# Optimization experiments

Measured on AMD Instinct MI355X. Metric: run time of the kernel, lower is better.

Reference implementation:

```python
import jax, jax.numpy as jnp
import numpy as np
from jax import lax

# config: B=8, T=32, input_chans=1, H=kernel_size=8, W=n_freq=256
# F1=32, F2=48, F3=256, F4=128, n_note=88, pooling_size=2, filter_size3=(3,64)
B, T, CIN, H, W = 8, 32, 1, 8, 256
F1, F2, F3, F4, NNOTE = 32, 48, 256, 128, 88


def _conv2d(x, w, b, padding):
    # x: (B, Cin, H, W), w: (Cout, Cin, kh, kw)
    y = lax.conv_general_dilated(x, w, (1, 1), padding,
                                 dimension_numbers=('NCHW', 'OIHW', 'NCHW'))
    return y + b[None, :, None, None]


def _clstm(x, w, b, F):
    # x: (B, C, T, H, W); ConvLSTM (no peephole, no LN), 'same' padding.
    xs = jnp.moveaxis(x, 2, 0)  # (T, B, C, H, W)
    h0 = jnp.zeros((x.shape[0], F, x.shape[3], x.shape[4]), x.dtype)
    c0 = h0

    def step(carry, xt):
        h, c = carry
        z = _conv2d(jnp.concatenate([xt, h], axis=1), w, b, 'SAME')
        i, f, g, o = jnp.split(z, 4, axis=1)
        c = jax.nn.sigmoid(f) * c + jax.nn.sigmoid(i) * jnp.tanh(g)
        h = jax.nn.sigmoid(o) * jnp.tanh(c)
        return (h, c), h

    _, hs = lax.scan(step, (h0, c0), xs)  # (T, B, F, H, W)
    return jnp.moveaxis(hs, 0, 2)  # (B, F, T, H, W)


def _maxpool3d(x):
    # MaxPool3d(kernel=2, stride=2) over (T, H, W) of a (B, C, T, H, W) tensor
    return lax.reduce_window(x, -jnp.inf, lax.max,
                             (1, 1, 2, 2, 2), (1, 1, 2, 2, 2), 'VALID')


def setup_inputs() -> dict:
    key = jax.random.key(0)
    ks = jax.random.split(key, 11)
    s = 0.05
    return {
        'x':  jax.random.normal(ks[0], (B, CIN, T, H, W), jnp.float32),
        'w1': jax.random.normal(ks[1], (4 * F1, CIN + F1, 3, 3), jnp.float32) * s,
        'b1': jnp.zeros((4 * F1,), jnp.float32),
        'w2': jax.random.normal(ks[2], (4 * F2, F1 + F2, 3, 3), jnp.float32) * s,
        'b2': jnp.zeros((4 * F2,), jnp.float32),
        'w3': jax.random.normal(ks[3], (F3, F2, 3, 64), jnp.float32) * s,
        'b3': jnp.zeros((F3,), jnp.float32),
        'w4': jax.random.normal(ks[4], (F4, F3, 1, 1), jnp.float32) * s,
        'b4': jnp.zeros((F4,), jnp.float32),
        'w5': jax.random.normal(ks[5], (NNOTE, F4, 1, 1), jnp.float32) * s,
        'b5': jnp.zeros((NNOTE,), jnp.float32),
    }


def reference(x, w1, b1, w2, b2, w3, b3, w4, b4, w5, b5):
    x = _clstm(x, w1, b1, F1)          # (B, F1, T, H, W)
    x = _maxpool3d(x)                  # (B, F1, T/2, H/2, W/2)
    x = _clstm(x, w2, b2, F2)          # (B, F2, T/2, H/2, W/2)
    x = _maxpool3d(x)                  # (B, F2, 8, 2, 64)
    x = x.reshape(B, F2, -1, 64)       # (B, F2, 16, 64), filter_size3[1]=64
    x = jax.nn.elu(_conv2d(x, w3, b3, 'VALID'))  # (B, F3, 14, 1); dropout=eval noop
    x = jax.nn.elu(_conv2d(x, w4, b4, 'VALID'))  # (B, F4, 14, 1)
    x = _conv2d(x, w5, b5, 'VALID')              # (B, 88, 14, 1)
    return x
```

## Files before the change

kernel.cpp:

```cpp
#include <hip/hip_runtime.h>
#include <math.h>


#define DEVINL static __device__ __forceinline__
typedef __attribute__((ext_vector_type(8))) short short8;
typedef __attribute__((ext_vector_type(4))) float f32x4;

#define PLANE_W3 2359296

DEVINL float sigm(float x) { return 1.0f / (1.0f + __expf(-x)); }
DEVINL float tanh_fast(float x) { return 1.0f - 2.0f / (__expf(2.0f * x) + 1.0f); }
DEVINL float elu(float x) { return x > 0.0f ? x : expm1f(x); }
DEVINL unsigned short bf16_rne(float v) {
    unsigned u = __float_as_uint(v);
    unsigned r = (u + 0x7FFF + ((u >> 16) & 1)) >> 16;
    return (unsigned short)r;
}
DEVINL float bf16_to_f(unsigned short h) { return __uint_as_float(((unsigned)h) << 16); }
DEVINL unsigned pack_hl(float v) {
    unsigned short hi = bf16_rne(v);
    unsigned short lo = bf16_rne(v - bf16_to_f(hi));
    return (unsigned)hi | ((unsigned)lo << 16);
}
DEVINL float upk(unsigned u) {
    return __uint_as_float(u << 16) + __uint_as_float(u & 0xffff0000u);
}

DEVINL void lstm1_body(
    int xq, int y, int b, int t,
    const unsigned* __restrict__ xpk, const unsigned short* __restrict__ w1F,
    const float* __restrict__ b1,
    const unsigned* __restrict__ hprev, const unsigned* __restrict__ hpool,
    unsigned* __restrict__ hout, float* __restrict__ c1,
    unsigned* __restrict__ p1pk)
{
    __shared__ __align__(16) unsigned short sBhi[34 * 128];
    __shared__ __align__(16) unsigned short sBlo[34 * 128];
    const int x0 = xq * 32;
    const int tid = threadIdx.x;

    if (((t & 1) == 0) && t >= 2 && (y & 1) == 1) {
        int tp = (t >> 1) - 1, yp = y >> 1;
        for (int e = tid; e < 512; e += 256) {
            int f = e >> 4, xl = e & 15;
            int xp = (x0 >> 1) + xl, gx = x0 + 2 * xl;
            int b0 = ((b * 32 + f) * 8 + (y - 1)) * 256 + gx;
            float m = upk(hpool[b0]);
            m = fmaxf(m, upk(hpool[b0 + 1]));
            m = fmaxf(m, upk(hpool[b0 + 256]));
            m = fmaxf(m, upk(hpool[b0 + 257]));
            m = fmaxf(m, upk(hprev[b0]));
            m = fmaxf(m, upk(hprev[b0 + 1]));
            m = fmaxf(m, upk(hprev[b0 + 256]));
            m = fmaxf(m, upk(hprev[b0 + 257]));
            p1pk[(((b * 32 + f) * 16 + tp) * 4 + yp) * 128 + xp] = pack_hl(m);
        }
    }

    for (int e = tid; e < 34 * 128; e += 256) {
        int lx = e % 34, kk = e / 34;
        unsigned u = 0;
        if (kk < 99) {
            int ci = kk / 3, dy = kk - ci * 3;
            int gy = y + dy - 1, gx = x0 + lx - 1;
            if (gy >= 0 && gy < 8 && gx >= 0 && gx < 256)
                u = (ci == 0) ? xpk[((b * 32 + t) * 8 + gy) * 256 + gx]
                              : hprev[((b * 32 + (ci - 1)) * 8 + gy) * 256 + gx];
        }
        int a16 = lx * 128 + (((kk >> 3) ^ (lx & 15)) << 3) + (kk & 7);
        sBhi[a16] = (unsigned short)u;
        sBlo[a16] = (unsigned short)(u >> 16);
    }
    __syncthreads();

    const int l = tid & 63;
    const int wv = __builtin_amdgcn_readfirstlane(tid >> 6);
    const int ln = l & 15, kg = l >> 4;
    f32x4 acc[2][2];
#pragma unroll
    for (int i = 0; i < 2; ++i)
#pragma unroll
        for (int j = 0; j < 2; ++j) acc[i][j] = (f32x4){0.f, 0.f, 0.f, 0.f};

#pragma unroll
    for (int kk = 0; kk < 4; ++kk) {
        short8 bh[2][3], bl[2][3];
#pragma unroll
        for (int ntl = 0; ntl < 2; ++ntl)
#pragma unroll
            for (int dx = 0; dx < 3; ++dx) {
                int lx = ntl * 16 + ln + dx;
                int slot = kk * 4 + kg;
                int boff = lx * 128 + ((slot ^ (lx & 15)) << 3);
                bh[ntl][dx] = *(const short8*)&sBhi[boff];
                bl[ntl][dx] = *(const short8*)&sBlo[boff];
            }
#pragma unroll
        for (int mtl = 0; mtl < 2; ++mtl)
#pragma unroll
            for (int dx = 0; dx < 3; ++dx) {
                int aoff = ((((dx * 8 + wv * 2 + mtl) * 4 + kk) * 4 + kg) * 16 + ln) * 8;
                short8 ah = *(const short8*)&w1F[aoff];
#pragma unroll
                for (int ntl = 0; ntl < 2; ++ntl) {
                    acc[mtl][ntl] = __builtin_amdgcn_mfma_f32_16x16x32_bf16(ah, bl[ntl][dx], acc[mtl][ntl], 0, 0, 0);
                    acc[mtl][ntl] = __builtin_amdgcn_mfma_f32_16x16x32_bf16(ah, bh[ntl][dx], acc[mtl][ntl], 0, 0, 0);
                }
            }
    }

#pragma unroll
    for (int mtl = 0; mtl < 2; ++mtl) {
        const int f = (wv * 2 + mtl) * 4 + kg;
        const float bi = b1[f], bff = b1[32 + f], bg = b1[64 + f], bo = b1[96 + f];
#pragma unroll
        for (int ntl = 0; ntl < 2; ++ntl) {
            f32x4 a = acc[mtl][ntl];
            int gidx = ((b * 32 + f) * 8 + y) * 256 + x0 + ntl * 16 + ln;
            float zi = a[0] + bi, zf = a[1] + bff, zg = a[2] + bg, zo = a[3] + bo;
            float cv = c1[gidx];
            float cn = sigm(zf) * cv + sigm(zi) * tanh_fast(zg);
            c1[gidx] = cn;
            hout[gidx] = pack_hl(sigm(zo) * tanh_fast(cn));
        }
    }
}

DEVINL void lstm2_body(
    int xq, int y, int b, int t,
    const unsigned* __restrict__ p1pk, const unsigned short* __restrict__ w2F,
    const float* __restrict__ b2,
    const unsigned* __restrict__ hprev, const unsigned* __restrict__ hpool,
    float* __restrict__ c2, unsigned* __restrict__ hout,
    unsigned short* __restrict__ p2hi, unsigned short* __restrict__ p2lo,
    const unsigned* __restrict__ h30, const unsigned* __restrict__ h31)
{
    __shared__ __align__(16) unsigned short sChi[18 * 256];
    __shared__ __align__(16) unsigned short sClo[18 * 256];
    const int x0 = xq * 16;
    const int tid = threadIdx.x;

    if (((t & 1) == 0) && t >= 2 && y < 2) {
        int tp = (t >> 1) - 1;
        for (int e = tid; e < 48 * 8; e += 256) {
            int f = e >> 3, xl = e & 7;
            int xp = xq * 8 + xl;
            int g0 = ((b * 48 + f) * 4 + y * 2) * 128 + xp * 2;
            float m = fmaxf(fmaxf(upk(hpool[g0]), upk(hpool[g0 + 1])),
                            fmaxf(upk(hpool[g0 + 128]), upk(hpool[g0 + 129])));
            m = fmaxf(m, fmaxf(fmaxf(upk(hprev[g0]), upk(hprev[g0 + 1])),
                               fmaxf(upk(hprev[g0 + 128]), upk(hprev[g0 + 129]))));
            int pi = ((b * 48 + f) * 16 + tp * 2 + y) * 64 + xp;
            unsigned pm = pack_hl(m);
            p2hi[pi] = (unsigned short)pm;
            p2lo[pi] = (unsigned short)(pm >> 16);
        }
    }

    for (int idx = tid; idx < 80 * 54; idx += 256) {
        int ci = idx / 54, rem = idx % 54;
        int dy = rem / 18, lx = rem % 18;
        int gy = y + dy - 1, gx = x0 + lx - 1;
        unsigned u = 0;
        if (gy >= 0 && gy < 4 && gx >= 0 && gx < 128) {
            if (ci < 32) {
                if (t == 15) {
                    int b0 = ((b * 32 + ci) * 8 + gy * 2) * 256 + gx * 2;
                    float m = upk(h30[b0]);
                    m = fmaxf(m, upk(h30[b0 + 1]));
                    m = fmaxf(m, upk(h30[b0 + 256]));
                    m = fmaxf(m, upk(h30[b0 + 257]));
                    m = fmaxf(m, upk(h31[b0]));
                    m = fmaxf(m, upk(h31[b0 + 1]));
                    m = fmaxf(m, upk(h31[b0 + 256]));
                    m = fmaxf(m, upk(h31[b0 + 257]));
                    u = pack_hl(m);
                } else {
                    u = p1pk[(((b * 32 + ci) * 16 + t) * 4 + gy) * 128 + gx];
                }
            } else {
                u = hprev[((b * 48 + (ci - 32)) * 4 + gy) * 128 + gx];
            }
        }
        int k = ci * 3 + dy;
        int a16 = lx * 256 + (((k >> 3) ^ (lx & 15)) << 3) + (k & 7);
        sChi[a16] = (unsigned short)u;
        sClo[a16] = (unsigned short)(u >> 16);
    }
    for (int e = tid; e < 18 * 16; e += 256) {
        int lx = e >> 4, k = 240 + (e & 15);
        int a16 = lx * 256 + (((k >> 3) ^ (lx & 15)) << 3) + (k & 7);
        sChi[a16] = 0;
        sClo[a16] = 0;
    }
    __syncthreads();

    const int l = tid & 63;
    const int wv = __builtin_amdgcn_readfirstlane(tid >> 6);
    const int ln = l & 15, kg = l >> 4;
    f32x4 acc[3] = {{0.f,0.f,0.f,0.f},{0.f,0.f,0.f,0.f},{0.f,0.f,0.f,0.f}};

#pragma unroll
    for (int kk = 0; kk < 8; ++kk) {
        short8 bh[3], bl[3];
#pragma unroll
        for (int dx = 0; dx < 3; ++dx) {
            int lx = ln + dx;
            int boff = lx * 256 + ((((kk << 2) + kg) ^ (lx & 15)) << 3);
            bh[dx] = *(const short8*)&sChi[boff];
            bl[dx] = *(const short8*)&sClo[boff];
        }
#pragma unroll
        for (int j = 0; j < 3; ++j) {
            int mt = wv * 3 + j;
#pragma unroll
            for (int dx = 0; dx < 3; ++dx) {
                int aoff = ((((dx * 12 + mt) * 8 + kk) * 4 + kg) * 16 + ln) * 8;
                short8 ah = *(const short8*)&w2F[aoff];
                acc[j] = __builtin_amdgcn_mfma_f32_16x16x32_bf16(ah, bl[dx], acc[j], 0, 0, 0);
                acc[j] = __builtin_amdgcn_mfma_f32_16x16x32_bf16(ah, bh[dx], acc[j], 0, 0, 0);
            }
        }
    }

    const int x = x0 + ln;
#pragma unroll
    for (int j = 0; j < 3; ++j) {
        int mt = wv * 3 + j;
        int f = mt * 4 + kg;
        float zi = acc[j][0] + b2[f];
        float zf = acc[j][1] + b2[48 + f];
        float zg = acc[j][2] + b2[96 + f];
        float zo = acc[j][3] + b2[144 + f];
        int gidx = ((b * 48 + f) * 4 + y) * 128 + x;
        float cv = c2[gidx];
        float cn = sigm(zf) * cv + sigm(zi) * tanh_fast(zg);
        c2[gidx] = cn;
        hout[gidx] = pack_hl(sigm(zo) * tanh_fast(cn));
    }
}

__global__ __launch_bounds__(256) void step_k(
    const unsigned* __restrict__ xpk, const unsigned short* __restrict__ w1F,
    const float* __restrict__ b1,
    const unsigned* __restrict__ hprev1, const unsigned* __restrict__ hpool1,
    unsigned* __restrict__ hout1, float* __restrict__ c1,
    unsigned* __restrict__ p1pk,
    const unsigned short* __restrict__ w2F, const float* __restrict__ b2,
    const unsigned* __restrict__ hprev2, const unsigned* __restrict__ hpool2,
    unsigned* __restrict__ hout2, float* __restrict__ c2,
    unsigned short* __restrict__ p2hi, unsigned short* __restrict__ p2lo,
    int t, int t2)
{
    int bid = blockIdx.x;
    if (gridDim.x == 768) {
        if (bid < 256) {
            lstm2_body(bid & 7, (bid >> 3) & 3, bid >> 5, t2,
                       p1pk, w2F, b2, hprev2, hpool2, c2, hout2, p2hi, p2lo,
                       hout1, hout1);
            return;
        }
        bid -= 256;
    }
    lstm1_body(bid & 7, (bid >> 3) & 7, bid >> 6, t,
               xpk, w1F, b1, hprev1, hpool1, hout1, c1, p1pk);
}

__global__ __launch_bounds__(256) void lstm2_k(
    const unsigned* __restrict__ p1pk, const unsigned short* __restrict__ w2F,
    const float* __restrict__ b2,
    const unsigned* __restrict__ hprev, const unsigned* __restrict__ hpool,
    float* __restrict__ c2, unsigned* __restrict__ hout,
    unsigned short* __restrict__ p2hi, unsigned short* __restrict__ p2lo,
    const unsigned* __restrict__ h30, const unsigned* __restrict__ h31, int t)
{
    int bid = blockIdx.x;
    lstm2_body(bid & 7, (bid >> 3) & 3, bid >> 5, t,
               p1pk, w2F, b2, hprev, hpool, c2, hout, p2hi, p2lo, h30, h31);
}

__global__ void pool2(const unsigned* __restrict__ hA, const unsigned* __restrict__ hB,
                      unsigned short* __restrict__ p2hi, unsigned short* __restrict__ p2lo,
                      int tp)
{
    int idx = blockIdx.x * 256 + threadIdx.x;
    if (idx >= 8 * 48 * 2 * 64) return;
    int xp = idx & 63;
    int t1 = idx >> 6;
    int yp = t1 & 1; t1 >>= 1;
    int f = t1 % 48, b = t1 / 48;
    float m = -INFINITY;
#pragma unroll
    for (int dy = 0; dy < 2; ++dy)
#pragma unroll
        for (int dx = 0; dx < 2; ++dx) {
            int g = ((b * 48 + f) * 4 + yp * 2 + dy) * 128 + xp * 2 + dx;
            m = fmaxf(m, fmaxf(upk(hA[g]), upk(hB[g])));
        }
    int pi = ((b * 48 + f) * 16 + tp * 2 + yp) * 64 + xp;
    unsigned pm = pack_hl(m);
    p2hi[pi] = (unsigned short)pm;
    p2lo[pi] = (unsigned short)(pm >> 16);
}

__global__ __launch_bounds__(256) void conv3_part(
    const unsigned short* __restrict__ p2hi, const unsigned short* __restrict__ p2lo,
    const unsigned short* __restrict__ w3F,
    float* __restrict__ part)
{
    __shared__ float sRed[4 * 7 * 256];
    const int mq = blockIdx.x, ck = blockIdx.y;
    const int tid = threadIdx.x;
    const int l = tid & 63;
    const int wv = __builtin_amdgcn_readfirstlane(tid >> 6);
    const int c = ck * 4 + wv;
    const int ln = l & 15, kg = l >> 4;

    int rowbase[7];
#pragma unroll
    for (int nt = 0; nt < 7; ++nt) {
        int col = nt * 16 + ln;
        int bi = col / 14, r = col % 14;
        rowbase[nt] = (bi * 48 + c) * 16 + r;
    }

    f32x4 acc[7];
#pragma unroll
    for (int nt = 0; nt < 7; ++nt) acc[nt] = (f32x4){0.f, 0.f, 0.f, 0.f};

#pragma unroll
    for (int kk = 0; kk < 6; ++kk) {
        int aoff = ((((mq * 48 + c) * 6 + kk) * 4 + kg) * 16 + ln) * 8;
        short8 ah = *(const short8*)&w3F[aoff];
        short8 al = *(const short8*)&w3F[PLANE_W3 + aoff];
        int s = kk * 4 + kg;
        int dr = s >> 3, w0 = (s & 7) * 8;
#pragma unroll
        for (int nt = 0; nt < 7; ++nt) {
            int boff = (rowbase[nt] + dr) * 64 + w0;
            short8 bh = *(const short8*)&p2hi[boff];
            short8 bl = *(const short8*)&p2lo[boff];
            acc[nt] = __builtin_amdgcn_mfma_f32_16x16x32_bf16(al, bh, acc[nt], 0, 0, 0);
            acc[nt] = __builtin_amdgcn_mfma_f32_16x16x32_bf16(ah, bl, acc[nt], 0, 0, 0);
            acc[nt] = __builtin_amdgcn_mfma_f32_16x16x32_bf16(ah, bh, acc[nt], 0, 0, 0);
        }
    }

#pragma unroll
    for (int nt = 0; nt < 7; ++nt)
        *(f32x4*)&sRed[wv * 1792 + nt * 256 + l * 4] = acc[nt];
    __syncthreads();

#pragma unroll
    for (int nt = 0; nt < 7; ++nt) {
        float s = sRed[nt * 256 + tid] + sRed[1792 + nt * 256 + tid] +
                  sRed[2 * 1792 + nt * 256 + tid] + sRed[3 * 1792 + nt * 256 + tid];
        int r16 = (tid >> 6) * 4 + (tid & 3);
        int m = mq * 16 + r16;
        int col = nt * 16 + ((tid >> 2) & 15);
        part[(ck * 256 + m) * 112 + col] = s;
    }
}

__global__ __launch_bounds__(256) void head(
    const float* __restrict__ part, const float* __restrict__ b3,
    const float* __restrict__ w4T, const float* __restrict__ b4,
    const float* __restrict__ w5T, const float* __restrict__ b5,
    float* __restrict__ out)
{
    __shared__ float sO3[256];
    __shared__ float sO4[128];
    const int col = blockIdx.x;
    const int b = col / 14, r = col % 14;
    const int tid = threadIdx.x;

    float s = b3[tid];
#pragma unroll
    for (int ck = 0; ck < 12; ++ck)
        s += part[(ck * 256 + tid) * 112 + col];
    sO3[tid] = elu(s);
    __syncthreads();

    if (tid < 128) {
        float a4 = b4[tid];
        for (int c = 0; c < 256; ++c)
            a4 = fmaf(sO3[c], w4T[c * 128 + tid], a4);
        sO4[tid] = elu(a4);
    }
    __syncthreads();

    if (tid < 88) {
        float a5 = b5[tid];
        for (int c = 0; c < 128; ++c)
            a5 = fmaf(sO4[c], w5T[c * 88 + tid], a5);
        out[(b * 88 + tid) * 14 + r] = a5;
    }
}

__global__ void prep(const float* __restrict__ x, const float* __restrict__ w1,
                     const float* __restrict__ w2, const float* __restrict__ w3,
                     const float* __restrict__ w4, const float* __restrict__ w5,
                     unsigned* __restrict__ zeroA,
                     unsigned* __restrict__ zeroB,
                     unsigned* __restrict__ xpk,
                     unsigned short* __restrict__ w1F, unsigned short* __restrict__ w2F,
                     unsigned short* __restrict__ w3F,
                     float* __restrict__ w4T, float* __restrict__ w5T)
{
    int i = blockIdx.x * 256 + threadIdx.x;
    if (i < 65536) {
        uint4 z = {0, 0, 0, 0};
        uint4* p = (uint4*)&zeroA[i * 16];
        p[0] = z; p[1] = z; p[2] = z; p[3] = z;
        return;
    }
    i -= 65536;
    if (i < 24576) {
        uint4 z = {0, 0, 0, 0};
        uint4* p = (uint4*)&zeroB[i * 16];
        p[0] = z; p[1] = z; p[2] = z; p[3] = z;
        return;
    }
    i -= 24576;
    if (i < 131072) {
        const float4 v = *(const float4*)&x[i * 4];
        uint4 o;
        o.x = pack_hl(v.x); o.y = pack_hl(v.y);
        o.z = pack_hl(v.z); o.w = pack_hl(v.w);
        *(uint4*)&xpk[i * 4] = o;
        return;
    }
    i -= 131072;
    if (i < 6144) {
        int base = i * 8;
        int dx = base / 16384, rem = base % 16384;
        int mt = rem / 2048, r2 = rem % 2048;
        int kk = r2 / 512, r3 = r2 % 512;
        int kg = r3 / 128, ln = (r3 % 128) / 8;
        int f = mt * 4 + (ln >> 2), gate = ln & 3;
        int co = gate * 32 + f;
        int k0 = kk * 32 + kg * 8;
        short8 h;
#pragma unroll
        for (int e = 0; e < 8; ++e) {
            int k = k0 + e;
            float v = (k < 99) ? w1[co * 297 + (k / 3) * 9 + (k % 3) * 3 + dx] : 0.0f;
            h[e] = (short)bf16_rne(v);
        }
        *(short8*)&w1F[base] = h;
        return;
    }
    i -= 6144;
    if (i < 18432) {
        int base = i * 8;
        int dx = base / 49152, rem = base % 49152;
        int mt = rem / 4096, r2 = rem % 4096;
        int kk = r2 / 512, r3 = r2 % 512;
        int kg = r3 / 128, ln = (r3 % 128) / 8;
        int f = mt * 4 + (ln >> 2), gate = ln & 3;
        int co = gate * 48 + f;
        int k0 = kk * 32 + kg * 8;
        short8 h;
#pragma unroll
        for (int e = 0; e < 8; ++e) {
            int k = k0 + e;
            float v = (k < 240) ? w2[co * 720 + (k / 3) * 9 + (k % 3) * 3 + dx] : 0.0f;
            h[e] = (short)bf16_rne(v);
        }
        *(short8*)&w2F[base] = h;
        return;
    }
    i -= 18432;
    if (i < 294912) {
        int base = i * 8;
        int mq = base / 147456, rem = base % 147456;
        int c = rem / 3072, r2 = rem % 3072;
        int kk = r2 / 512, r3 = r2 % 512;
        int kg = r3 / 128, ln = (r3 % 128) / 8;
        int m = mq * 16 + ln;
        int kc0 = kk * 32 + kg * 8;
        int dr = kc0 >> 6, w0 = kc0 & 63;
        const float* src = &w3[((m * 48 + c) * 3 + dr) * 64 + w0];
        short8 hh, hl;
#pragma unroll
        for (int e = 0; e < 8; ++e) {
            float v = src[e];
            unsigned short hi = bf16_rne(v);
            hh[e] = (short)hi;
            hl[e] = (short)bf16_rne(v - bf16_to_f(hi));
        }
        *(short8*)&w3F[base] = hh;
        *(short8*)&w3F[PLANE_W3 + base] = hl;
        return;
    }
    i -= 294912;
    if (i < 32768) {
        int n = i / 256, cch = i % 256;
        w4T[cch * 128 + n] = w4[i];
        return;
    }
    i -= 32768;
    if (i < 11264) {
        int n = i / 128, cch = i % 128;
        w5T[cch * 88 + n] = w5[i];
    }
}

extern "C" void kernel_launch(void* const* d_in, const int* in_sizes, int n_in,
                              void* d_out, int out_size, void* d_ws, size_t ws_size,
                              hipStream_t stream)
{
    const float* x  = (const float*)d_in[0];
    const float* w1 = (const float*)d_in[1];
    const float* b1 = (const float*)d_in[2];
    const float* w2 = (const float*)d_in[3];
    const float* b2 = (const float*)d_in[4];
    const float* w3 = (const float*)d_in[5];
    const float* b3 = (const float*)d_in[6];
    const float* w4 = (const float*)d_in[7];
    const float* b4 = (const float*)d_in[8];
    const float* w5 = (const float*)d_in[9];
    const float* b5 = (const float*)d_in[10];
    float* out = (float*)d_out;

    float* ws = (float*)d_ws;
    size_t off = 0;
    auto alloc = [&](size_t n) { float* p = ws + off; off += n; return p; };
    unsigned* h1[3];
    h1[0] = (unsigned*)alloc(524288); h1[1] = (unsigned*)alloc(524288);
    h1[2] = (unsigned*)alloc(524288);
    float* c1 = alloc(524288);
    unsigned* xpk = (unsigned*)alloc(524288);
    unsigned* p1pk = (unsigned*)alloc(2097152);
    unsigned* h2[3];
    h2[0] = (unsigned*)alloc(196608); h2[1] = (unsigned*)alloc(196608);
    h2[2] = (unsigned*)alloc(196608);
    float* c2 = alloc(196608);
    unsigned short* p2hi = (unsigned short*)alloc(196608);
    unsigned short* p2lo = (unsigned short*)alloc(196608);
    float* part = alloc(344064);
    unsigned short* w1F = (unsigned short*)alloc(24576);
    unsigned short* w2F = (unsigned short*)alloc(73728);
    unsigned short* w3F = (unsigned short*)alloc(2359296);
    float* w4T = alloc(32768);
    float* w5T = alloc(11264);
    (void)ws_size; (void)off;

    prep<<<2284, 256, 0, stream>>>(x, w1, w2, w3, w4, w5,
                                   h1[2], h2[2], xpk, w1F, w2F, w3F, w4T, w5T);

    for (int t = 0; t < 32; ++t) {
        int t2 = ((t & 1) == 0 && t >= 4) ? (t - 4) / 2 : (t == 31 ? 14 : -1);
        int nblk = (t2 >= 0) ? 768 : 512;
        step_k<<<nblk, 256, 0, stream>>>(
            xpk, w1F, b1, h1[(t + 2) % 3], h1[(t + 1) % 3], h1[t % 3], c1, p1pk,
            w2F, b2,
            t2 >= 0 ? h2[(t2 + 2) % 3] : h2[0],
            t2 >= 0 ? h2[(t2 + 1) % 3] : h2[0],
            t2 >= 0 ? h2[t2 % 3] : h2[0],
            c2, p2hi, p2lo, t, t2);
    }

    lstm2_k<<<256, 256, 0, stream>>>(p1pk, w2F, b2, h2[2], h2[1], c2, h2[0],
                                     p2hi, p2lo, h1[0], h1[1], 15);
    pool2<<<192, 256, 0, stream>>>(h2[2], h2[0], p2hi, p2lo, 7);

    conv3_part<<<dim3(16, 12), 256, 0, stream>>>(p2hi, p2lo, w3F, part);
    head<<<112, 256, 0, stream>>>(part, b3, w4T, b4, w5T, b5, out);
}
```

Baseline: 484.6 us.

## Fold weight prep into first LSTM step and drop state zeroing and x packing

The big prep kernel is split up. A tiny prep1 packs only w1, and the w2/w3/w4/w5 repacking runs as extra blocks of the t=0 step kernel, overlapping the first LSTM1 step. The zero-fill of the h/c buffers is removed: at t=0 the code skips hprev loads and treats c as zero. The input x is now hi/lo-split on the fly inside the LSTM1 tile load instead of through a precomputed xpk buffer. This removes a serial prep launch and memory traffic, at the cost of extra pack work every step and a larger t=0 grid.

After: 505.3 us. 1.04x slower.

```diff
diff --git a/kernel.cpp b/kernel.cpp
--- a/kernel.cpp
+++ b/kernel.cpp
@@ -28,7 +28,7 @@
 
 DEVINL void lstm1_body(
     int xq, int y, int b, int t,
-    const unsigned* __restrict__ xpk, const unsigned short* __restrict__ w1F,
+    const float* __restrict__ x, const unsigned short* __restrict__ w1F,
     const float* __restrict__ b1,
     const unsigned* __restrict__ hprev, const unsigned* __restrict__ hpool,
     unsigned* __restrict__ hout, float* __restrict__ c1,
@@ -63,9 +63,12 @@
         if (kk < 99) {
             int ci = kk / 3, dy = kk - ci * 3;
             int gy = y + dy - 1, gx = x0 + lx - 1;
-            if (gy >= 0 && gy < 8 && gx >= 0 && gx < 256)
-                u = (ci == 0) ? xpk[((b * 32 + t) * 8 + gy) * 256 + gx]
-                              : hprev[((b * 32 + (ci - 1)) * 8 + gy) * 256 + gx];
+            if (gy >= 0 && gy < 8 && gx >= 0 && gx < 256) {
+                if (ci == 0)
+                    u = pack_hl(x[((b * 32 + t) * 8 + gy) * 256 + gx]);
+                else if (t > 0)
+                    u = hprev[((b * 32 + (ci - 1)) * 8 + gy) * 256 + gx];
+            }
         }
         int a16 = lx * 128 + (((kk >> 3) ^ (lx & 15)) << 3) + (kk & 7);
         sBhi[a16] = (unsigned short)u;
@@ -118,7 +121,7 @@
             f32x4 a = acc[mtl][ntl];
             int gidx = ((b * 32 + f) * 8 + y) * 256 + x0 + ntl * 16 + ln;
             float zi = a[0] + bi, zf = a[1] + bff, zg = a[2] + bg, zo = a[3] + bo;
-            float cv = c1[gidx];
+            float cv = (t > 0) ? c1[gidx] : 0.0f;
             float cn = sigm(zf) * cv + sigm(zi) * tanh_fast(zg);
             c1[gidx] = cn;
             hout[gidx] = pack_hl(sigm(zo) * tanh_fast(cn));
@@ -178,7 +181,7 @@
                 } else {
                     u = p1pk[(((b * 32 + ci) * 16 + t) * 4 + gy) * 128 + gx];
                 }
-            } else {
+            } else if (t > 0) {
                 u = hprev[((b * 48 + (ci - 32)) * 4 + gy) * 128 + gx];
             }
         }
@@ -233,226 +236,22 @@
         float zg = acc[j][2] + b2[96 + f];
         float zo = acc[j][3] + b2[144 + f];
         int gidx = ((b * 48 + f) * 4 + y) * 128 + x;
-        float cv = c2[gidx];
+        float cv = (t > 0) ? c2[gidx] : 0.0f;
         float cn = sigm(zf) * cv + sigm(zi) * tanh_fast(zg);
         c2[gidx] = cn;
         hout[gidx] = pack_hl(sigm(zo) * tanh_fast(cn));
     }
 }
 
-__global__ __launch_bounds__(256) void step_k(
-    const unsigned* __restrict__ xpk, const unsigned short* __restrict__ w1F,
-    const float* __restrict__ b1,
-    const unsigned* __restrict__ hprev1, const unsigned* __restrict__ hpool1,
-    unsigned* __restrict__ hout1, float* __restrict__ c1,
-    unsigned* __restrict__ p1pk,
-    const unsigned short* __restrict__ w2F, const float* __restrict__ b2,
-    const unsigned* __restrict__ hprev2, const unsigned* __restrict__ hpool2,
-    unsigned* __restrict__ hout2, float* __restrict__ c2,
-    unsigned short* __restrict__ p2hi, unsigned short* __restrict__ p2lo,
-    int t, int t2)
-{
-    int bid = blockIdx.x;
-    if (gridDim.x == 768) {
-        if (bid < 256) {
-            lstm2_body(bid & 7, (bid >> 3) & 3, bid >> 5, t2,
-                       p1pk, w2F, b2, hprev2, hpool2, c2, hout2, p2hi, p2lo,
-                       hout1, hout1);
-            return;
-        }
-        bid -= 256;
-    }
-    lstm1_body(bid & 7, (bid >> 3) & 7, bid >> 6, t,
-               xpk, w1F, b1, hprev1, hpool1, hout1, c1, p1pk);
-}
-
-__global__ __launch_bounds__(256) void lstm2_k(
-    const unsigned* __restrict__ p1pk, const unsigned short* __restrict__ w2F,
-    const float* __restrict__ b2,
-    const unsigned* __restrict__ hprev, const unsigned* __restrict__ hpool,
-    float* __restrict__ c2, unsigned* __restrict__ hout,
-    unsigned short* __restrict__ p2hi, unsigned short* __restrict__ p2lo,
-    const unsigned* __restrict__ h30, const unsigned* __restrict__ h31, int t)
-{
-    int bid = blockIdx.x;
-    lstm2_body(bid & 7, (bid >> 3) & 3, bid >> 5, t,
-               p1pk, w2F, b2, hprev, hpool, c2, hout, p2hi, p2lo, h30, h31);
-}
-
-__global__ void pool2(const unsigned* __restrict__ hA, const unsigned* __restrict__ hB,
-                      unsigned short* __restrict__ p2hi, unsigned short* __restrict__ p2lo,
-                      int tp)
-{
-    int idx = blockIdx.x * 256 + threadIdx.x;
-    if (idx >= 8 * 48 * 2 * 64) return;
-    int xp = idx & 63;
-    int t1 = idx >> 6;
-    int yp = t1 & 1; t1 >>= 1;
-    int f = t1 % 48, b = t1 / 48;
-    float m = -INFINITY;
-#pragma unroll
-    for (int dy = 0; dy < 2; ++dy)
-#pragma unroll
-        for (int dx = 0; dx < 2; ++dx) {
-            int g = ((b * 48 + f) * 4 + yp * 2 + dy) * 128 + xp * 2 + dx;
-            m = fmaxf(m, fmaxf(upk(hA[g]), upk(hB[g])));
-        }
-    int pi = ((b * 48 + f) * 16 + tp * 2 + yp) * 64 + xp;
-    unsigned pm = pack_hl(m);
-    p2hi[pi] = (unsigned short)pm;
-    p2lo[pi] = (unsigned short)(pm >> 16);
-}
-
-__global__ __launch_bounds__(256) void conv3_part(
-    const unsigned short* __restrict__ p2hi, const unsigned short* __restrict__ p2lo,
-    const unsigned short* __restrict__ w3F,
-    float* __restrict__ part)
-{
-    __shared__ float sRed[4 * 7 * 256];
-    const int mq = blockIdx.x, ck = blockIdx.y;
-    const int tid = threadIdx.x;
-    const int l = tid & 63;
-    const int wv = __builtin_amdgcn_readfirstlane(tid >> 6);
-    const int c = ck * 4 + wv;
-    const int ln = l & 15, kg = l >> 4;
-
-    int rowbase[7];
-#pragma unroll
-    for (int nt = 0; nt < 7; ++nt) {
-        int col = nt * 16 + ln;
-        int bi = col / 14, r = col % 14;
-        rowbase[nt] = (bi * 48 + c) * 16 + r;
-    }
-
-    f32x4 acc[7];
-#pragma unroll
-    for (int nt = 0; nt < 7; ++nt) acc[nt] = (f32x4){0.f, 0.f, 0.f, 0.f};
-
-#pragma unroll
-    for (int kk = 0; kk < 6; ++kk) {
-        int aoff = ((((mq * 48 + c) * 6 + kk) * 4 + kg) * 16 + ln) * 8;
-        short8 ah = *(const short8*)&w3F[aoff];
-        short8 al = *(const short8*)&w3F[PLANE_W3 + aoff];
-        int s = kk * 4 + kg;
-        int dr = s >> 3, w0 = (s & 7) * 8;
-#pragma unroll
-        for (int nt = 0; nt < 7; ++nt) {
-            int boff = (rowbase[nt] + dr) * 64 + w0;
-            short8 bh = *(const short8*)&p2hi[boff];
-            short8 bl = *(const short8*)&p2lo[boff];
-            acc[nt] = __builtin_amdgcn_mfma_f32_16x16x32_bf16(al, bh, acc[nt], 0, 0, 0);
-            acc[nt] = __builtin_amdgcn_mfma_f32_16x16x32_bf16(ah, bl, acc[nt], 0, 0, 0);
-            acc[nt] = __builtin_amdgcn_mfma_f32_16x16x32_bf16(ah, bh, acc[nt], 0, 0, 0);
-        }
-    }
-
-#pragma unroll
-    for (int nt = 0; nt < 7; ++nt)
-        *(f32x4*)&sRed[wv * 1792 + nt * 256 + l * 4] = acc[nt];
-    __syncthreads();
-
-#pragma unroll
-    for (int nt = 0; nt < 7; ++nt) {
-        float s = sRed[nt * 256 + tid] + sRed[1792 + nt * 256 + tid] +
-                  sRed[2 * 1792 + nt * 256 + tid] + sRed[3 * 1792 + nt * 256 + tid];
-        int r16 = (tid >> 6) * 4 + (tid & 3);
-        int m = mq * 16 + r16;
-        int col = nt * 16 + ((tid >> 2) & 15);
-        part[(ck * 256 + m) * 112 + col] = s;
-    }
-}
-
-__global__ __launch_bounds__(256) void head(
-    const float* __restrict__ part, const float* __restrict__ b3,
-    const float* __restrict__ w4T, const float* __restrict__ b4,
-    const float* __restrict__ w5T, const float* __restrict__ b5,
-    float* __restrict__ out)
-{
-    __shared__ float sO3[256];
-    __shared__ float sO4[128];
-    const int col = blockIdx.x;
-    const int b = col / 14, r = col % 14;
-    const int tid = threadIdx.x;
-
-    float s = b3[tid];
-#pragma unroll
-    for (int ck = 0; ck < 12; ++ck)
-        s += part[(ck * 256 + tid) * 112 + col];
-    sO3[tid] = elu(s);
-    __syncthreads();
-
-    if (tid < 128) {
-        float a4 = b4[tid];
-        for (int c = 0; c < 256; ++c)
-            a4 = fmaf(sO3[c], w4T[c * 128 + tid], a4);
-        sO4[tid] = elu(a4);
-    }
-    __syncthreads();
-
-    if (tid < 88) {
-        float a5 = b5[tid];
-        for (int c = 0; c < 128; ++c)
-            a5 = fmaf(sO4[c], w5T[c * 88 + tid], a5);
-        out[(b * 88 + tid) * 14 + r] = a5;
-    }
-}
-
-__global__ void prep(const float* __restrict__ x, const float* __restrict__ w1,
-                     const float* __restrict__ w2, const float* __restrict__ w3,
-                     const float* __restrict__ w4, const float* __restrict__ w5,
-                     unsigned* __restrict__ zeroA,
-                     unsigned* __restrict__ zeroB,
-                     unsigned* __restrict__ xpk,
-                     unsigned short* __restrict__ w1F, unsigned short* __restrict__ w2F,
-                     unsigned short* __restrict__ w3F,
-                     float* __restrict__ w4T, float* __restrict__ w5T)
-{
-    int i = blockIdx.x * 256 + threadIdx.x;
-    if (i < 65536) {
-        uint4 z = {0, 0, 0, 0};
-        uint4* p = (uint4*)&zeroA[i * 16];
-        p[0] = z; p[1] = z; p[2] = z; p[3] = z;
-        return;
-    }
-    i -= 65536;
-    if (i < 24576) {
-        uint4 z = {0, 0, 0, 0};
-        uint4* p = (uint4*)&zeroB[i * 16];
-        p[0] = z; p[1] = z; p[2] = z; p[3] = z;
-        return;
-    }
-    i -= 24576;
-    if (i < 131072) {
-        const float4 v = *(const float4*)&x[i * 4];
-        uint4 o;
-        o.x = pack_hl(v.x); o.y = pack_hl(v.y);
-        o.z = pack_hl(v.z); o.w = pack_hl(v.w);
-        *(uint4*)&xpk[i * 4] = o;
-        return;
-    }
-    i -= 131072;
-    if (i < 6144) {
-        int base = i * 8;
-        int dx = base / 16384, rem = base % 16384;
-        int mt = rem / 2048, r2 = rem % 2048;
-        int kk = r2 / 512, r3 = r2 % 512;
-        int kg = r3 / 128, ln = (r3 % 128) / 8;
-        int f = mt * 4 + (ln >> 2), gate = ln & 3;
-        int co = gate * 32 + f;
-        int k0 = kk * 32 + kg * 8;
-        short8 h;
-#pragma unroll
-        for (int e = 0; e < 8; ++e) {
-            int k = k0 + e;
-            float v = (k < 99) ? w1[co * 297 + (k / 3) * 9 + (k % 3) * 3 + dx] : 0.0f;
-            h[e] = (short)bf16_rne(v);
-        }
-        *(short8*)&w1F[base] = h;
-        return;
-    }
-    i -= 6144;
-    if (i < 18432) {
-        int base = i * 8;
+DEVINL void prep2_body(
+    int p,
+    const float* __restrict__ w2, const float* __restrict__ w3,
+    const float* __restrict__ w4, const float* __restrict__ w5,
+    unsigned short* __restrict__ w2F, unsigned short* __restrict__ w3F,
+    float* __restrict__ w4T, float* __restrict__ w5T)
+{
+    if (p < 18432) {
+        int base = p * 8;
         int dx = base / 49152, rem = base % 49152;
         int mt = rem / 4096, r2 = rem % 4096;
         int kk = r2 / 512, r3 = r2 % 512;
@@ -470,9 +269,9 @@
         *(short8*)&w2F[base] = h;
         return;
     }
-    i -= 18432;
-    if (i < 294912) {
-        int base = i * 8;
+    p -= 18432;
+    if (p < 294912) {
+        int base = p * 8;
         int mq = base / 147456, rem = base % 147456;
         int c = rem / 3072, r2 = rem % 3072;
         int kk = r2 / 512, r3 = r2 % 512;
@@ -493,17 +292,204 @@
         *(short8*)&w3F[PLANE_W3 + base] = hl;
         return;
     }
-    i -= 294912;
-    if (i < 32768) {
-        int n = i / 256, cch = i % 256;
-        w4T[cch * 128 + n] = w4[i];
+    p -= 294912;
+    if (p < 32768) {
+        int n = p / 256, cch = p % 256;
+        w4T[cch * 128 + n] = w4[p];
         return;
     }
-    i -= 32768;
-    if (i < 11264) {
-        int n = i / 128, cch = i % 128;
-        w5T[cch * 88 + n] = w5[i];
-    }
+    p -= 32768;
+    if (p < 11264) {
+        int n = p / 128, cch = p % 128;
+        w5T[cch * 88 + n] = w5[p];
+    }
+}
+
+__global__ __launch_bounds__(256) void step_k(
+    const float* __restrict__ x, const unsigned short* __restrict__ w1F,
+    const float* __restrict__ b1,
+    const unsigned* __restrict__ hprev1, const unsigned* __restrict__ hpool1,
+    unsigned* __restrict__ hout1, float* __restrict__ c1,
+    unsigned* __restrict__ p1pk,
+    const unsigned short* __restrict__ w2F, const float* __restrict__ b2,
+    const unsigned* __restrict__ hprev2, const unsigned* __restrict__ hpool2,
+    unsigned* __restrict__ hout2, float* __restrict__ c2,
+    unsigned short* __restrict__ p2hi, unsigned short* __restrict__ p2lo,
+    const float* __restrict__ w2, const float* __restrict__ w3,
+    const float* __restrict__ w4, const float* __restrict__ w5,
+    unsigned short* __restrict__ w2Fw, unsigned short* __restrict__ w3F,
+    float* __restrict__ w4T, float* __restrict__ w5T,
+    int t, int t2)
+{
+    int bid = blockIdx.x;
+    if (t2 >= 0) {
+        if (bid < 256) {
+            lstm2_body(bid & 7, (bid >> 3) & 3, bid >> 5, t2,
+                       p1pk, w2F, b2, hprev2, hpool2, c2, hout2, p2hi, p2lo,
+                       hout1, hout1);
+            return;
+        }
+        bid -= 256;
+    } else if (bid >= 512) {
+        prep2_body((bid - 512) * 256 + threadIdx.x, w2, w3, w4, w5,
+                   w2Fw, w3F, w4T, w5T);
+        return;
+    }
+    lstm1_body(bid & 7, (bid >> 3) & 7, bid >> 6, t,
+               x, w1F, b1, hprev1, hpool1, hout1, c1, p1pk);
+}
+
+__global__ __launch_bounds__(256) void lstm2_k(
+    const unsigned* __restrict__ p1pk, const unsigned short* __restrict__ w2F,
+    const float* __restrict__ b2,
+    const unsigned* __restrict__ hprev, const unsigned* __restrict__ hpool,
+    float* __restrict__ c2, unsigned* __restrict__ hout,
+    unsigned short* __restrict__ p2hi, unsigned short* __restrict__ p2lo,
+    const unsigned* __restrict__ h30, const unsigned* __restrict__ h31, int t)
+{
+    int bid = blockIdx.x;
+    lstm2_body(bid & 7, (bid >> 3) & 3, bid >> 5, t,
+               p1pk, w2F, b2, hprev, hpool, c2, hout, p2hi, p2lo, h30, h31);
+}
+
+__global__ void pool2(const unsigned* __restrict__ hA, const unsigned* __restrict__ hB,
+                      unsigned short* __restrict__ p2hi, unsigned short* __restrict__ p2lo,
+                      int tp)
+{
+    int idx = blockIdx.x * 256 + threadIdx.x;
+    if (idx >= 8 * 48 * 2 * 64) return;
+    int xp = idx & 63;
+    int t1 = idx >> 6;
+    int yp = t1 & 1; t1 >>= 1;
+    int f = t1 % 48, b = t1 / 48;
+    float m = -INFINITY;
+#pragma unroll
+    for (int dy = 0; dy < 2; ++dy)
+#pragma unroll
+        for (int dx = 0; dx < 2; ++dx) {
+            int g = ((b * 48 + f) * 4 + yp * 2 + dy) * 128 + xp * 2 + dx;
+            m = fmaxf(m, fmaxf(upk(hA[g]), upk(hB[g])));
+        }
+    int pi = ((b * 48 + f) * 16 + tp * 2 + yp) * 64 + xp;
+    unsigned pm = pack_hl(m);
+    p2hi[pi] = (unsigned short)pm;
+    p2lo[pi] = (unsigned short)(pm >> 16);
+}
+
+__global__ __launch_bounds__(256) void conv3_part(
+    const unsigned short* __restrict__ p2hi, const unsigned short* __restrict__ p2lo,
+    const unsigned short* __restrict__ w3F,
+    float* __restrict__ part)
+{
+    __shared__ float sRed[4 * 7 * 256];
+    const int mq = blockIdx.x, ck = blockIdx.y;
+    const int tid = threadIdx.x;
+    const int l = tid & 63;
+    const int wv = __builtin_amdgcn_readfirstlane(tid >> 6);
+    const int c = ck * 4 + wv;
+    const int ln = l & 15, kg = l >> 4;
+
+    int rowbase[7];
+#pragma unroll
+    for (int nt = 0; nt < 7; ++nt) {
+        int col = nt * 16 + ln;
+        int bi = col / 14, r = col % 14;
+        rowbase[nt] = (bi * 48 + c) * 16 + r;
+    }
+
+    f32x4 acc[7];
+#pragma unroll
+    for (int nt = 0; nt < 7; ++nt) acc[nt] = (f32x4){0.f, 0.f, 0.f, 0.f};
+
+#pragma unroll
+    for (int kk = 0; kk < 6; ++kk) {
+        int aoff = ((((mq * 48 + c) * 6 + kk) * 4 + kg) * 16 + ln) * 8;
+        short8 ah = *(const short8*)&w3F[aoff];
+        short8 al = *(const short8*)&w3F[PLANE_W3 + aoff];
+        int s = kk * 4 + kg;
+        int dr = s >> 3, w0 = (s & 7) * 8;
+#pragma unroll
+        for (int nt = 0; nt < 7; ++nt) {
+            int boff = (rowbase[nt] + dr) * 64 + w0;
+            short8 bh = *(const short8*)&p2hi[boff];
+            short8 bl = *(const short8*)&p2lo[boff];
+            acc[nt] = __builtin_amdgcn_mfma_f32_16x16x32_bf16(al, bh, acc[nt], 0, 0, 0);
+            acc[nt] = __builtin_amdgcn_mfma_f32_16x16x32_bf16(ah, bl, acc[nt], 0, 0, 0);
+            acc[nt] = __builtin_amdgcn_mfma_f32_16x16x32_bf16(ah, bh, acc[nt], 0, 0, 0);
+        }
+    }
+
+#pragma unroll
+    for (int nt = 0; nt < 7; ++nt)
+        *(f32x4*)&sRed[wv * 1792 + nt * 256 + l * 4] = acc[nt];
+    __syncthreads();
+
+#pragma unroll
+    for (int nt = 0; nt < 7; ++nt) {
+        float s = sRed[nt * 256 + tid] + sRed[1792 + nt * 256 + tid] +
+                  sRed[2 * 1792 + nt * 256 + tid] + sRed[3 * 1792 + nt * 256 + tid];
+        int r16 = (tid >> 6) * 4 + (tid & 3);
+        int m = mq * 16 + r16;
+        int col = nt * 16 + ((tid >> 2) & 15);
+        part[(ck * 256 + m) * 112 + col] = s;
+    }
+}
+
+__global__ __launch_bounds__(256) void head(
+    const float* __restrict__ part, const float* __restrict__ b3,
+    const float* __restrict__ w4T, const float* __restrict__ b4,
+    const float* __restrict__ w5T, const float* __restrict__ b5,
+    float* __restrict__ out)
+{
+    __shared__ float sO3[256];
+    __shared__ float sO4[128];
+    const int col = blockIdx.x;
+    const int b = col / 14, r = col % 14;
+    const int tid = threadIdx.x;
+
+    float s = b3[tid];
+#pragma unroll
+    for (int ck = 0; ck < 12; ++ck)
+        s += part[(ck * 256 + tid) * 112 + col];
+    sO3[tid] = elu(s);
+    __syncthreads();
+
+    if (tid < 128) {
+        float a4 = b4[tid];
+        for (int c = 0; c < 256; ++c)
+            a4 = fmaf(sO3[c], w4T[c * 128 + tid], a4);
+        sO4[tid] = elu(a4);
+    }
+    __syncthreads();
+
+    if (tid < 88) {
+        float a5 = b5[tid];
+        for (int c = 0; c < 128; ++c)
+            a5 = fmaf(sO4[c], w5T[c * 88 + tid], a5);
+        out[(b * 88 + tid) * 14 + r] = a5;
+    }
+}
+
+__global__ void prep1(const float* __restrict__ w1, unsigned short* __restrict__ w1F)
+{
+    int i = blockIdx.x * 256 + threadIdx.x;
+    if (i >= 6144) return;
+    int base = i * 8;
+    int dx = base / 16384, rem = base % 16384;
+    int mt = rem / 2048, r2 = rem % 2048;
+    int kk = r2 / 512, r3 = r2 % 512;
+    int kg = r3 / 128, ln = (r3 % 128) / 8;
+    int f = mt * 4 + (ln >> 2), gate = ln & 3;
+    int co = gate * 32 + f;
+    int k0 = kk * 32 + kg * 8;
+    short8 h;
+#pragma unroll
+    for (int e = 0; e < 8; ++e) {
+        int k = k0 + e;
+        float v = (k < 99) ? w1[co * 297 + (k / 3) * 9 + (k % 3) * 3 + dx] : 0.0f;
+        h[e] = (short)bf16_rne(v);
+    }
+    *(short8*)&w1F[base] = h;
 }
 
 extern "C" void kernel_launch(void* const* d_in, const int* in_sizes, int n_in,
@@ -530,7 +516,6 @@
     h1[0] = (unsigned*)alloc(524288); h1[1] = (unsigned*)alloc(524288);
     h1[2] = (unsigned*)alloc(524288);
     float* c1 = alloc(524288);
-    unsigned* xpk = (unsigned*)alloc(524288);
     unsigned* p1pk = (unsigned*)alloc(2097152);
     unsigned* h2[3];
     h2[0] = (unsigned*)alloc(196608); h2[1] = (unsigned*)alloc(196608);
@@ -546,19 +531,20 @@
     float* w5T = alloc(11264);
     (void)ws_size; (void)off;
 
-    prep<<<2284, 256, 0, stream>>>(x, w1, w2, w3, w4, w5,
-                                   h1[2], h2[2], xpk, w1F, w2F, w3F, w4T, w5T);
+    prep1<<<24, 256, 0, stream>>>(w1, w1F);
 
     for (int t = 0; t < 32; ++t) {
         int t2 = ((t & 1) == 0 && t >= 4) ? (t - 4) / 2 : (t == 31 ? 14 : -1);
-        int nblk = (t2 >= 0) ? 768 : 512;
+        int nblk = (t2 >= 0) ? 768 : (t == 0 ? 1908 : 512);
         step_k<<<nblk, 256, 0, stream>>>(
-            xpk, w1F, b1, h1[(t + 2) % 3], h1[(t + 1) % 3], h1[t % 3], c1, p1pk,
+            x, w1F, b1, h1[(t + 2) % 3], h1[(t + 1) % 3], h1[t % 3], c1, p1pk,
             w2F, b2,
             t2 >= 0 ? h2[(t2 + 2) % 3] : h2[0],
             t2 >= 0 ? h2[(t2 + 1) % 3] : h2[0],
             t2 >= 0 ? h2[t2 % 3] : h2[0],
-            c2, p2hi, p2lo, t, t2);
+            c2, p2hi, p2lo,
+            w2, w3, w4, w5, w2F, w3F, w4T, w5T,
+            t, t2);
     }
 
     lstm2_k<<<256, 256, 0, stream>>>(p1pk, w2F, b2, h2[2], h2[1], c2, h2[0],
```
